# Performance work log

Measured on AMD Instinct MI355X. Metric: run time of the kernel, lower is better.

The kernel has to match this reference:

```python
import jax, jax.numpy as jnp
import numpy as np
from jax import lax

UP = 4          # upscale_factor (pixel_shuffle factor hardcoded to 4 in ReconBlock)
OUT_CH = UP * UP * 5 * 5  # 400
MID_CH = UP * 5           # 20


def setup_inputs() -> dict:
    key = jax.random.key(0)
    ks = jax.random.split(key, 5)
    B, A, H, W = 2, 5, 96, 96
    pic = jax.random.uniform(ks[0], (B, A, A, H, W), dtype=jnp.float32)
    w1 = jax.random.normal(ks[1], (OUT_CH, 1, 5, 5, 9, 9), dtype=jnp.float32) * 0.02
    b1 = jnp.zeros((OUT_CH,), jnp.float32)
    w2a = jax.random.normal(ks[2], (MID_CH, 1, 3, 3, 5, 5), dtype=jnp.float32) * 0.02
    b2a = jnp.zeros((MID_CH,), jnp.float32)
    w2b = jax.random.normal(ks[3], (OUT_CH, MID_CH, 3, 3, 5, 5), dtype=jnp.float32) * 0.02
    b2b = jnp.zeros((OUT_CH,), jnp.float32)
    return {"pic": pic, "w1": w1, "b1": b1, "w2a": w2a, "b2a": b2a,
            "w2b": w2b, "b2b": b2b}


def _conv4d(x, w):
    # x: [B, Cin, A1, A2, H, W], w: [Cout, Cin, k1, k2, k3, k4], VALID, stride 1
    return lax.conv_general_dilated(x, w, window_strides=(1, 1, 1, 1),
                                    padding='VALID')


def _bias(b):
    return b[None, :, None, None, None, None]


def reference(pic, w1, b1, w2a, b2a, w2b, b2b):
    B, A1, A2, H, W = pic.shape
    # Padder: pad H,W by 4 each side with value 0.5
    padded = jnp.full((B, A1, A2, H + 8, W + 8), 0.5, dtype=pic.dtype)
    padded = padded.at[:, :, :, 4:-4, 4:-4].set(pic)
    x = padded[:, None]  # [B,1,A1,A2,H+8,W+8]

    # DimBlock_1: single 4D conv (5,5,9,9); ReLU defined but never applied
    p1 = _conv4d(x, w1) + _bias(b1)              # [B,400,1,1,H,W]

    # DimBlock_2: two 4D convs (3,3,5,5) with ReLU
    buf = jax.nn.relu(_conv4d(x, w2a) + _bias(b2a))   # [B,20,3,3,H+4,W+4]
    p2 = jax.nn.relu(_conv4d(buf, w2b) + _bias(b2b))  # [B,400,1,1,H,W]

    # BottleNeck
    mid = (p1 + p2) / 2                           # [B,400,1,1,H,W]

    # ReconBlock: take angular position (0,0), pixel_shuffle(4), split 25 -> 5x5
    y = mid[:, :, 0, 0]                           # [B,400,H,W]
    Bc, C, Hh, Ww = y.shape
    r = 4
    y = y.reshape(Bc, 25, r, r, Hh, Ww)
    y = y.transpose(0, 1, 4, 2, 5, 3).reshape(Bc, 25, Hh * r, Ww * r)
    return y.reshape(Bc, 5, 5, Hh * r, Ww * r)
```

## Files before the change

kernel.cpp:

```cpp
#include <hip/hip_runtime.h>
#include <hip/hip_bf16.h>


typedef __attribute__((ext_vector_type(8))) unsigned short ushort8;
typedef __attribute__((ext_vector_type(8))) __bf16 bf16x8;
typedef __attribute__((ext_vector_type(4))) float f32x4;

#define NB 2
#define HSLOT 576
#define HBUF (4 * HSLOT * 8)
#define WST 14336

static __device__ __forceinline__ unsigned short f2bf(float f) {
    __hip_bfloat16 h = __float2bfloat16(f);
    return *reinterpret_cast<unsigned short*>(&h);
}
static __device__ __forceinline__ void gload16(const unsigned short* g, unsigned short* l) {
    __builtin_amdgcn_global_load_lds(
        (const __attribute__((address_space(1))) unsigned int*)(const void*)g,
        (__attribute__((address_space(3))) unsigned int*)(void*)l, 16, 0, 0);
}

__global__ __launch_bounds__(256) void prep_fused_kernel(
    const float* __restrict__ pic, const float* __restrict__ w1,
    const float* __restrict__ w2a, const float* __restrict__ w2b,
    unsigned short* __restrict__ Pn, unsigned short* __restrict__ Wp,
    unsigned short* __restrict__ Wc2) {
    __shared__ unsigned short sT[28544];
    const int blk = blockIdx.x;
    const int tid = threadIdx.x;

    if (blk < 85) {
        int idx = blk * 256 + tid;
        if (idx >= NB * 104 * 104) return;
        int x = idx % 104;
        int y = (idx / 104) % 104;
        int b = idx / (104 * 104);
        unsigned short vals[32];
        bool inter = (y >= 4 && y < 100 && x >= 4 && x < 100);
#pragma unroll
        for (int c = 0; c < 25; ++c) {
            float v = inter ? pic[((b * 25 + c) * 96 + (y - 4)) * 96 + (x - 4)] : 0.5f;
            vals[c] = f2bf(v);
        }
#pragma unroll
        for (int c = 25; c < 32; ++c) vals[c] = 0;
        ushort8* dst = (ushort8*)(Pn + idx * 32);
#pragma unroll
        for (int j = 0; j < 4; ++j) dst[j] = *(ushort8*)&vals[j * 8];
    } else if (blk < 127) {
        int b2 = blk - 85;
        int ocB = b2 % 7, cc = b2 / 7;
        for (int n32 = 0; n32 < 2; ++n32) {
            for (int j = 0; j < 4; ++j) {
                int p  = tid * 4 + j;
                int gl = p >> 5, ol = p & 31;
                int oc = ocB * 64 + n32 * 32 + ol;
                int gp = cc * 32 + gl;
                const float* src = nullptr;
                if (oc < 400 && gp < 180) {
                    int mc = gp % 20, uv = gp / 20;
                    src = w2b + oc * 4500 + (mc * 9 + uv) * 25;
                }
#pragma unroll
                for (int tap = 0; tap < 25; ++tap)
                    sT[(gl * 25 + tap) * 33 + ol] = src ? f2bf(src[tap]) : (unsigned short)0;
            }
            __syncthreads();
            for (int i = 0; i < 13; ++i) {
                int sid = i * 256 + tid;
                if (sid < 3200) {
                    int tap = sid >> 7;
                    int r   = sid & 127;
                    int nb = r >> 6, lane = r & 63;
                    int kq = lane >> 4;
                    int olw = nb * 16 + (lane & 15);
                    unsigned short v8[8];
#pragma unroll
                    for (int e = 0; e < 8; ++e)
                        v8[e] = sT[((kq * 8 + e) * 25 + tap) * 33 + olw];
                    size_t d = (size_t)(cc * 25 + tap) * WST + ocB * 2048 +
                               (n32 * 2 + nb) * 512 + lane * 8;
                    *(ushort8*)(Wp + d) = *(ushort8*)v8;
                }
            }
            __syncthreads();
        }
    } else if (blk < 148) {
        int b3 = blk - 127;
        int ocB = b3 % 7, tt = b3 / 7;
        for (int n32 = 0; n32 < 2; ++n32) {
            for (int j = 0; j < 4; ++j) {
                int p  = tid * 4 + j;
                int cl = p >> 5, ol = p & 31;
                int oc = ocB * 64 + n32 * 32 + ol;
                const float* src = (oc < 400 && cl < 25)
                                       ? (w1 + oc * 2025 + cl * 81 + tt * 27) : nullptr;
#pragma unroll
                for (int tl = 0; tl < 27; ++tl)
                    sT[(cl * 27 + tl) * 33 + ol] = src ? f2bf(src[tl]) : (unsigned short)0;
            }
            __syncthreads();
            for (int i = 0; i < 14; ++i) {
                int sid = i * 256 + tid;
                if (sid < 3456) {
                    int tl = sid >> 7;
                    int r  = sid & 127;
                    int nb = r >> 6, lane = r & 63;
                    int kq = lane >> 4;
                    int olw = nb * 16 + (lane & 15);
                    unsigned short v8[8];
#pragma unroll
                    for (int e = 0; e < 8; ++e)
                        v8[e] = sT[((kq * 8 + e) * 27 + tl) * 33 + olw];
                    int tap_lin = tt * 27 + tl;
                    int dy = tap_lin / 9, dx = tap_lin % 9;
                    int tp = (dx < 5) ? (dy * 5 + dx) : (45 + dy * 4 + (dx - 5));
                    size_t d = (size_t)(150 + tp) * WST + ocB * 2048 +
                               (n32 * 2 + nb) * 512 + lane * 8;
                    *(ushort8*)(Wp + d) = *(ushort8*)v8;
                }
            }
            __syncthreads();
        }
    } else if (blk < 154) {
        int ocB2 = blk - 148;
        if (tid < 128) {
            int lane = tid & 63;
            int oc = ocB2 * 32 + (tid >> 6) * 16 + (lane & 15);
            int kb = (lane >> 4) * 8;
            int uv = oc / 20, mc = oc % 20;
            int u = uv / 3, v = uv % 3;
            const float* wb[8];
#pragma unroll
            for (int e = 0; e < 8; ++e) {
                int k  = kb + e;
                int c1 = k / 5, c2 = k % 5;
                int da1 = c1 - u, da2 = c2 - v;
                bool valid = (oc < 180) && ((unsigned)da1 < 3u) && ((unsigned)da2 < 3u);
                wb[e] = valid ? (w2a + mc * 225 + (da1 * 3 + da2) * 25) : (const float*)0;
            }
            for (int tap = 0; tap < 25; ++tap) {
                unsigned short fr[8];
#pragma unroll
                for (int e = 0; e < 8; ++e) fr[e] = wb[e] ? f2bf(wb[e][tap]) : (unsigned short)0;
                *(ushort8*)(Wc2 + ((size_t)(ocB2 * 25 + tap) * 128 + tid) * 8) = *(ushort8*)fr;
            }
        }
    }
}

__global__ __launch_bounds__(256) void conv2a_mfma_kernel(
    const unsigned short* __restrict__ Pn, const unsigned short* __restrict__ Wc2,
    const float* __restrict__ b2a, unsigned short* __restrict__ Bn) {
    __shared__ __align__(16) unsigned short sHalo[4 * 448 * 8];

    const int tid  = threadIdx.x;
    const int lane = tid & 63, w = tid >> 6;
    const int l15  = lane & 15, lhi = lane >> 4;
    const int gx0  = blockIdx.x;
    const int b    = gx0 / 52, t52 = gx0 % 52;
    const int ty0  = (t52 >> 2) * 8;
    const int tx0  = (t52 & 3) * 32;
    const int ocB  = blockIdx.y;

    for (int L2 = 0; L2 < 7; ++L2) {
        int p = L2 * 64 + lane;
        if (p >= 432) p = 0;
        int hy = (p * 58255) >> 21, hx = p - hy * 36;
        int gy = ty0 + hy; gy = gy > 103 ? 103 : gy;
        int gx = tx0 + hx; gx = gx > 103 ? 103 : gx;
        gload16(Pn + ((size_t)((b * 104 + gy) * 104 + gx)) * 32 + w * 8,
                &sHalo[(w * 448 + L2 * 64) * 8]);
    }
    float bs[2];
#pragma unroll
    for (int n = 0; n < 2; ++n) {
        int oc = ocB * 32 + n * 16 + l15;
        bs[n] = (oc < 180) ? b2a[oc % 20] : 0.f;
    }
    __syncthreads();

    const unsigned short* hb = &sHalo[(lhi * 448 + w * 72 + l15) * 8];
    const unsigned short* wq = Wc2 + (size_t)ocB * 25600 + lane * 8;

    f32x4 acc[4][2] = {};
#pragma unroll
    for (int t = 0; t < 25; ++t) {
        const int u = ((t / 5) * 36 + (t % 5)) * 8;
        bf16x8 a0 = *(const bf16x8*)(hb + u);
        bf16x8 a1 = *(const bf16x8*)(hb + u + 128);
        bf16x8 a2 = *(const bf16x8*)(hb + u + 288);
        bf16x8 a3 = *(const bf16x8*)(hb + u + 416);
        bf16x8 c0 = *(const bf16x8*)(wq);
        bf16x8 c1 = *(const bf16x8*)(wq + 512);
        __builtin_amdgcn_s_setprio(1);
        acc[0][0] = __builtin_amdgcn_mfma_f32_16x16x32_bf16(a0, c0, acc[0][0], 0, 0, 0);
        acc[0][1] = __builtin_amdgcn_mfma_f32_16x16x32_bf16(a0, c1, acc[0][1], 0, 0, 0);
        acc[1][0] = __builtin_amdgcn_mfma_f32_16x16x32_bf16(a1, c0, acc[1][0], 0, 0, 0);
        acc[1][1] = __builtin_amdgcn_mfma_f32_16x16x32_bf16(a1, c1, acc[1][1], 0, 0, 0);
        acc[2][0] = __builtin_amdgcn_mfma_f32_16x16x32_bf16(a2, c0, acc[2][0], 0, 0, 0);
        acc[2][1] = __builtin_amdgcn_mfma_f32_16x16x32_bf16(a2, c1, acc[2][1], 0, 0, 0);
        acc[3][0] = __builtin_amdgcn_mfma_f32_16x16x32_bf16(a3, c0, acc[3][0], 0, 0, 0);
        acc[3][1] = __builtin_amdgcn_mfma_f32_16x16x32_bf16(a3, c1, acc[3][1], 0, 0, 0);
        __builtin_amdgcn_s_setprio(0);
        wq += 1024;
    }

#pragma unroll
    for (int n = 0; n < 2; ++n) {
        int oc = ocB * 32 + n * 16 + l15;
#pragma unroll
        for (int m = 0; m < 4; ++m) {
            int y = ty0 + w * 2 + (m >> 1);
            if (y >= 100) continue;
            int x0 = tx0 + (m & 1) * 16 + lhi * 4;
#pragma unroll
            for (int i = 0; i < 4; ++i) {
                int x = x0 + i;
                if (x >= 100) continue;
                Bn[((size_t)((b * 100 + y) * 100 + x)) * 192 + oc] =
                    f2bf(fmaxf(acc[m][n][i] + bs[n], 0.f));
            }
        }
    }
}

#define MFMA16(A0, A1, A2, A3, B0, B1, B2, B3)                                          \
    {                                                                                   \
        __builtin_amdgcn_s_setprio(1);                                                  \
        acc[0][0] = __builtin_amdgcn_mfma_f32_16x16x32_bf16(A0, B0, acc[0][0], 0, 0, 0);\
        acc[0][1] = __builtin_amdgcn_mfma_f32_16x16x32_bf16(A0, B1, acc[0][1], 0, 0, 0);\
        acc[0][2] = __builtin_amdgcn_mfma_f32_16x16x32_bf16(A0, B2, acc[0][2], 0, 0, 0);\
        acc[0][3] = __builtin_amdgcn_mfma_f32_16x16x32_bf16(A0, B3, acc[0][3], 0, 0, 0);\
        acc[1][0] = __builtin_amdgcn_mfma_f32_16x16x32_bf16(A1, B0, acc[1][0], 0, 0, 0);\
        acc[1][1] = __builtin_amdgcn_mfma_f32_16x16x32_bf16(A1, B1, acc[1][1], 0, 0, 0);\
        acc[1][2] = __builtin_amdgcn_mfma_f32_16x16x32_bf16(A1, B2, acc[1][2], 0, 0, 0);\
        acc[1][3] = __builtin_amdgcn_mfma_f32_16x16x32_bf16(A1, B3, acc[1][3], 0, 0, 0);\
        acc[2][0] = __builtin_amdgcn_mfma_f32_16x16x32_bf16(A2, B0, acc[2][0], 0, 0, 0);\
        acc[2][1] = __builtin_amdgcn_mfma_f32_16x16x32_bf16(A2, B1, acc[2][1], 0, 0, 0);\
        acc[2][2] = __builtin_amdgcn_mfma_f32_16x16x32_bf16(A2, B2, acc[2][2], 0, 0, 0);\
        acc[2][3] = __builtin_amdgcn_mfma_f32_16x16x32_bf16(A2, B3, acc[2][3], 0, 0, 0);\
        acc[3][0] = __builtin_amdgcn_mfma_f32_16x16x32_bf16(A3, B0, acc[3][0], 0, 0, 0);\
        acc[3][1] = __builtin_amdgcn_mfma_f32_16x16x32_bf16(A3, B1, acc[3][1], 0, 0, 0);\
        acc[3][2] = __builtin_amdgcn_mfma_f32_16x16x32_bf16(A3, B2, acc[3][2], 0, 0, 0);\
        acc[3][3] = __builtin_amdgcn_mfma_f32_16x16x32_bf16(A3, B3, acc[3][3], 0, 0, 0);\
        __builtin_amdgcn_s_setprio(0);                                                  \
    }

__global__ __launch_bounds__(256, 2) void conv_mfma_kernel(
    const unsigned short* __restrict__ Pn, const unsigned short* __restrict__ Bn,
    const unsigned short* __restrict__ Wp, const float* __restrict__ b1,
    const float* __restrict__ b2b, float* __restrict__ out) {
    __shared__ __align__(16) unsigned short sHalo[2 * HBUF];

    const int tid  = threadIdx.x;
    const int lane = tid & 63, w = tid >> 6;
    const int l15  = lane & 15, lhi = lane >> 4;
    const int ocB  = blockIdx.y;
    const int pb   = blockIdx.x;
    const int b    = pb / 36;
    const int t36  = pb % 36;
    const int ty0  = (t36 / 3) * 8;
    const int tx0  = (t36 % 3) * 32;

    const int vA = (lhi * HSLOT + w * 72 + l15) * 8;

    auto stageA = [&](int cc, int par) {
        unsigned short* dst0 = &sHalo[par * HBUF + w * HSLOT * 8];
        for (int L2 = 0; L2 < 7; ++L2) {
            int p = L2 * 64 + lane;
            if (p >= 432) p = 0;
            int hy = (p * 58255) >> 21, hx = p - hy * 36;
            gload16(Bn + ((size_t)((b * 100 + ty0 + hy) * 100 + tx0 + hx)) * 192 +
                        cc * 32 + w * 8,
                    dst0 + L2 * 512);
        }
    };
    auto stageB = [&](int seg, int par) {
        int cx = tx0 + (seg == 7 ? 5 : 0);
        unsigned short* dst0 = &sHalo[par * HBUF + w * HSLOT * 8];
        for (int L2 = 0; L2 < 9; ++L2) {
            int p = L2 * 64 + lane;
            int hy = (p * 58255) >> 21, hx = p - hy * 36;
            int gx = cx + hx;
            gx = gx > 103 ? 103 : gx;
            gload16(Pn + ((size_t)((b * 104 + ty0 + hy) * 104 + gx)) * 32 + w * 8,
                    dst0 + L2 * 512);
        }
    };

    float bb2[4], bb1[4];
#pragma unroll
    for (int n = 0; n < 4; ++n) {
        int oc  = ocB * 64 + n * 16 + l15;
        int occ = oc < 400 ? oc : 399;
        bb2[n] = b2b[occ];
        bb1[n] = b1[occ];
    }

    const unsigned short* wq = Wp + ocB * 2048 + lane * 8;
    bf16x8 c0 = *(const bf16x8*)(wq);
    bf16x8 c1 = *(const bf16x8*)(wq + 512);
    bf16x8 c2 = *(const bf16x8*)(wq + 1024);
    bf16x8 c3 = *(const bf16x8*)(wq + 1536);
    stageA(0, 0);
    __syncthreads();

    f32x4 acc[4][4] = {};
    bf16x8 a0, a1, a2, a3, q0, q1, q2, q3, n0, n1, n2, n3;

    for (int cc = 0; cc < 6; ++cc) {
        const unsigned short* hb = &sHalo[(cc & 1) * HBUF + vA];
        a0 = *(const bf16x8*)(hb);
        a1 = *(const bf16x8*)(hb + 128);
        a2 = *(const bf16x8*)(hb + 288);
        a3 = *(const bf16x8*)(hb + 416);
        if (cc < 5) stageA(cc + 1, (cc + 1) & 1);
        else        stageB(6, 0);
#pragma unroll
        for (int t = 0; t < 25; ++t) {
            wq += WST;
            n0 = *(const bf16x8*)(wq);
            n1 = *(const bf16x8*)(wq + 512);
            n2 = *(const bf16x8*)(wq + 1024);
            n3 = *(const bf16x8*)(wq + 1536);
            if (t < 24) {
                const int u = (((t + 1) / 5) * 36 + ((t + 1) % 5)) * 8;
                q0 = *(const bf16x8*)(hb + u);
                q1 = *(const bf16x8*)(hb + u + 128);
                q2 = *(const bf16x8*)(hb + u + 288);
                q3 = *(const bf16x8*)(hb + u + 416);
            }
            MFMA16(a0, a1, a2, a3, c0, c1, c2, c3);
            c0 = n0; c1 = n1; c2 = n2; c3 = n3;
            if (t < 24) { a0 = q0; a1 = q1; a2 = q2; a3 = q3; }
        }
        if (cc == 5) {
#pragma unroll
            for (int m = 0; m < 4; ++m)
#pragma unroll
                for (int n = 0; n < 4; ++n)
#pragma unroll
                    for (int i = 0; i < 4; ++i)
                        acc[m][n][i] = fmaxf(acc[m][n][i] + bb2[n], 0.f);
        }
        asm volatile("s_waitcnt vmcnt(4)" ::: "memory");
        asm volatile("s_barrier" ::: "memory");
    }

    {
        const unsigned short* hb = &sHalo[vA];
        a0 = *(const bf16x8*)(hb);
        a1 = *(const bf16x8*)(hb + 128);
        a2 = *(const bf16x8*)(hb + 288);
        a3 = *(const bf16x8*)(hb + 416);
        stageB(7, 1);
#pragma unroll
        for (int t = 0; t < 45; ++t) {
            wq += WST;
            n0 = *(const bf16x8*)(wq);
            n1 = *(const bf16x8*)(wq + 512);
            n2 = *(const bf16x8*)(wq + 1024);
            n3 = *(const bf16x8*)(wq + 1536);
            if (t < 44) {
                const int u = (((t + 1) / 5) * 36 + ((t + 1) % 5)) * 8;
                q0 = *(const bf16x8*)(hb + u);
                q1 = *(const bf16x8*)(hb + u + 128);
                q2 = *(const bf16x8*)(hb + u + 288);
                q3 = *(const bf16x8*)(hb + u + 416);
            }
            MFMA16(a0, a1, a2, a3, c0, c1, c2, c3);
            c0 = n0; c1 = n1; c2 = n2; c3 = n3;
            if (t < 44) { a0 = q0; a1 = q1; a2 = q2; a3 = q3; }
        }
        asm volatile("s_waitcnt vmcnt(4)" ::: "memory");
        asm volatile("s_barrier" ::: "memory");
    }

    {
        const unsigned short* hb = &sHalo[HBUF + vA];
        a0 = *(const bf16x8*)(hb);
        a1 = *(const bf16x8*)(hb + 128);
        a2 = *(const bf16x8*)(hb + 288);
        a3 = *(const bf16x8*)(hb + 416);
#pragma unroll
        for (int t = 0; t < 36; ++t) {
            if (t < 35) {
                wq += WST;
                n0 = *(const bf16x8*)(wq);
                n1 = *(const bf16x8*)(wq + 512);
                n2 = *(const bf16x8*)(wq + 1024);
                n3 = *(const bf16x8*)(wq + 1536);
                const int u = (((t + 1) / 4) * 36 + ((t + 1) % 4)) * 8;
                q0 = *(const bf16x8*)(hb + u);
                q1 = *(const bf16x8*)(hb + u + 128);
                q2 = *(const bf16x8*)(hb + u + 288);
                q3 = *(const bf16x8*)(hb + u + 416);
            }
            MFMA16(a0, a1, a2, a3, c0, c1, c2, c3);
            if (t < 35) { a0 = q0; a1 = q1; a2 = q2; a3 = q3;
                          c0 = n0; c1 = n1; c2 = n2; c3 = n3; }
        }
    }

#pragma unroll
    for (int n = 0; n < 4; ++n) {
        int oc = ocB * 64 + n * 16 + l15;
        if (oc >= 400) continue;
        float bv = bb1[n];
        int c25 = oc >> 4, r1 = (oc >> 2) & 3, r2 = oc & 3;
#pragma unroll
        for (int m = 0; m < 4; ++m) {
            int y  = ty0 + w * 2 + (m >> 1);
            int x0 = tx0 + (m & 1) * 16 + lhi * 4;
#pragma unroll
            for (int i = 0; i < 4; ++i) {
                out[((size_t)(b * 25 + c25) * 384 + y * 4 + r1) * 384 + (x0 + i) * 4 + r2] =
                    (acc[m][n][i] + bv) * 0.5f;
            }
        }
    }
}

extern "C" void kernel_launch(void* const* d_in, const int* in_sizes, int n_in,
                              void* d_out, int out_size, void* d_ws, size_t ws_size,
                              hipStream_t stream) {
    const float* pic = (const float*)d_in[0];
    const float* w1  = (const float*)d_in[1];
    const float* b1  = (const float*)d_in[2];
    const float* w2a = (const float*)d_in[3];
    const float* b2a = (const float*)d_in[4];
    const float* w2b = (const float*)d_in[5];
    const float* b2b = (const float*)d_in[6];
    float* out = (float*)d_out;

    char* ws = (char*)d_ws;
    unsigned short* Pn  = (unsigned short*)(ws);
    unsigned short* Bn  = (unsigned short*)(ws + 1384448);
    unsigned short* Wp  = (unsigned short*)(ws + 9064448);
    unsigned short* Wc2 = (unsigned short*)(ws + 15687680);

    prep_fused_kernel<<<154, 256, 0, stream>>>(pic, w1, w2a, w2b, Pn, Wp, Wc2);
    conv2a_mfma_kernel<<<dim3(104, 6), 256, 0, stream>>>(Pn, Wc2, b2a, Bn);
    conv_mfma_kernel<<<dim3(72, 7), 256, 0, stream>>>(Pn, Bn, Wp, b1, b2b, out);
}
```

Measured before the change: 149.2 us.

## Move big weight repacking into conv2a launch to overlap with conv2a compute

The w2b and w1 weight repacking moves out of the prep kernel and into extra blocks of the conv2a kernel, so the prep kernel only handles the input padding and the small w2a repack. The repack blocks now process 16 output channels per pass with a smaller shared buffer, which lets them share LDS with the conv2a halo tile. The intent is to shorten the serial prep stage and run the weight transform alongside the conv2a MFMA work. The cost is a heterogeneous kernel whose repack blocks may take longer than the conv blocks and so set the tail.

Result: slower. 159.4 us (+6.8%).

```diff
diff --git a/kernel.cpp b/kernel.cpp
--- a/kernel.cpp
+++ b/kernel.cpp
@@ -21,15 +21,11 @@
         (__attribute__((address_space(3))) unsigned int*)(void*)l, 16, 0, 0);
 }
 
-__global__ __launch_bounds__(256) void prep_fused_kernel(
-    const float* __restrict__ pic, const float* __restrict__ w1,
-    const float* __restrict__ w2a, const float* __restrict__ w2b,
-    unsigned short* __restrict__ Pn, unsigned short* __restrict__ Wp,
-    unsigned short* __restrict__ Wc2) {
-    __shared__ unsigned short sT[28544];
+__global__ __launch_bounds__(256) void prep1_kernel(
+    const float* __restrict__ pic, const float* __restrict__ w2a,
+    unsigned short* __restrict__ Pn, unsigned short* __restrict__ Wc2) {
     const int blk = blockIdx.x;
     const int tid = threadIdx.x;
-
     if (blk < 85) {
         int idx = blk * 256 + tid;
         if (idx >= NB * 104 * 104) return;
@@ -48,83 +44,8 @@
         ushort8* dst = (ushort8*)(Pn + idx * 32);
 #pragma unroll
         for (int j = 0; j < 4; ++j) dst[j] = *(ushort8*)&vals[j * 8];
-    } else if (blk < 127) {
-        int b2 = blk - 85;
-        int ocB = b2 % 7, cc = b2 / 7;
-        for (int n32 = 0; n32 < 2; ++n32) {
-            for (int j = 0; j < 4; ++j) {
-                int p  = tid * 4 + j;
-                int gl = p >> 5, ol = p & 31;
-                int oc = ocB * 64 + n32 * 32 + ol;
-                int gp = cc * 32 + gl;
-                const float* src = nullptr;
-                if (oc < 400 && gp < 180) {
-                    int mc = gp % 20, uv = gp / 20;
-                    src = w2b + oc * 4500 + (mc * 9 + uv) * 25;
-                }
-#pragma unroll
-                for (int tap = 0; tap < 25; ++tap)
-                    sT[(gl * 25 + tap) * 33 + ol] = src ? f2bf(src[tap]) : (unsigned short)0;
-            }
-            __syncthreads();
-            for (int i = 0; i < 13; ++i) {
-                int sid = i * 256 + tid;
-                if (sid < 3200) {
-                    int tap = sid >> 7;
-                    int r   = sid & 127;
-                    int nb = r >> 6, lane = r & 63;
-                    int kq = lane >> 4;
-                    int olw = nb * 16 + (lane & 15);
-                    unsigned short v8[8];
-#pragma unroll
-                    for (int e = 0; e < 8; ++e)
-                        v8[e] = sT[((kq * 8 + e) * 25 + tap) * 33 + olw];
-                    size_t d = (size_t)(cc * 25 + tap) * WST + ocB * 2048 +
-                               (n32 * 2 + nb) * 512 + lane * 8;
-                    *(ushort8*)(Wp + d) = *(ushort8*)v8;
-                }
-            }
-            __syncthreads();
-        }
-    } else if (blk < 148) {
-        int b3 = blk - 127;
-        int ocB = b3 % 7, tt = b3 / 7;
-        for (int n32 = 0; n32 < 2; ++n32) {
-            for (int j = 0; j < 4; ++j) {
-                int p  = tid * 4 + j;
-                int cl = p >> 5, ol = p & 31;
-                int oc = ocB * 64 + n32 * 32 + ol;
-                const float* src = (oc < 400 && cl < 25)
-                                       ? (w1 + oc * 2025 + cl * 81 + tt * 27) : nullptr;
-#pragma unroll
-                for (int tl = 0; tl < 27; ++tl)
-                    sT[(cl * 27 + tl) * 33 + ol] = src ? f2bf(src[tl]) : (unsigned short)0;
-            }
-            __syncthreads();
-            for (int i = 0; i < 14; ++i) {
-                int sid = i * 256 + tid;
-                if (sid < 3456) {
-                    int tl = sid >> 7;
-                    int r  = sid & 127;
-                    int nb = r >> 6, lane = r & 63;
-                    int kq = lane >> 4;
-                    int olw = nb * 16 + (lane & 15);
-                    unsigned short v8[8];
-#pragma unroll
-                    for (int e = 0; e < 8; ++e)
-                        v8[e] = sT[((kq * 8 + e) * 27 + tl) * 33 + olw];
-                    int tap_lin = tt * 27 + tl;
-                    int dy = tap_lin / 9, dx = tap_lin % 9;
-                    int tp = (dx < 5) ? (dy * 5 + dx) : (45 + dy * 4 + (dx - 5));
-                    size_t d = (size_t)(150 + tp) * WST + ocB * 2048 +
-                               (n32 * 2 + nb) * 512 + lane * 8;
-                    *(ushort8*)(Wp + d) = *(ushort8*)v8;
-                }
-            }
-            __syncthreads();
-        }
-    } else if (blk < 154) {
-        int ocB2 = blk - 148;
+    } else {
+        int ocB2 = blk - 85;
         if (tid < 128) {
             int lane = tid & 63;
             int oc = ocB2 * 32 + (tid >> 6) * 16 + (lane & 15);
@@ -150,77 +71,153 @@
     }
 }
 
-__global__ __launch_bounds__(256) void conv2a_mfma_kernel(
+__global__ __launch_bounds__(256) void conv2a_fused_kernel(
     const unsigned short* __restrict__ Pn, const unsigned short* __restrict__ Wc2,
-    const float* __restrict__ b2a, unsigned short* __restrict__ Bn) {
-    __shared__ __align__(16) unsigned short sHalo[4 * 448 * 8];
-
-    const int tid  = threadIdx.x;
-    const int lane = tid & 63, w = tid >> 6;
-    const int l15  = lane & 15, lhi = lane >> 4;
-    const int gx0  = blockIdx.x;
-    const int b    = gx0 / 52, t52 = gx0 % 52;
-    const int ty0  = (t52 >> 2) * 8;
-    const int tx0  = (t52 & 3) * 32;
-    const int ocB  = blockIdx.y;
-
-    for (int L2 = 0; L2 < 7; ++L2) {
-        int p = L2 * 64 + lane;
-        if (p >= 432) p = 0;
-        int hy = (p * 58255) >> 21, hx = p - hy * 36;
-        int gy = ty0 + hy; gy = gy > 103 ? 103 : gy;
-        int gx = tx0 + hx; gx = gx > 103 ? 103 : gx;
-        gload16(Pn + ((size_t)((b * 104 + gy) * 104 + gx)) * 32 + w * 8,
-                &sHalo[(w * 448 + L2 * 64) * 8]);
-    }
-    float bs[2];
-#pragma unroll
-    for (int n = 0; n < 2; ++n) {
-        int oc = ocB * 32 + n * 16 + l15;
-        bs[n] = (oc < 180) ? b2a[oc % 20] : 0.f;
-    }
-    __syncthreads();
-
-    const unsigned short* hb = &sHalo[(lhi * 448 + w * 72 + l15) * 8];
-    const unsigned short* wq = Wc2 + (size_t)ocB * 25600 + lane * 8;
-
-    f32x4 acc[4][2] = {};
-#pragma unroll
-    for (int t = 0; t < 25; ++t) {
-        const int u = ((t / 5) * 36 + (t % 5)) * 8;
-        bf16x8 a0 = *(const bf16x8*)(hb + u);
-        bf16x8 a1 = *(const bf16x8*)(hb + u + 128);
-        bf16x8 a2 = *(const bf16x8*)(hb + u + 288);
-        bf16x8 a3 = *(const bf16x8*)(hb + u + 416);
-        bf16x8 c0 = *(const bf16x8*)(wq);
-        bf16x8 c1 = *(const bf16x8*)(wq + 512);
-        __builtin_amdgcn_s_setprio(1);
-        acc[0][0] = __builtin_amdgcn_mfma_f32_16x16x32_bf16(a0, c0, acc[0][0], 0, 0, 0);
-        acc[0][1] = __builtin_amdgcn_mfma_f32_16x16x32_bf16(a0, c1, acc[0][1], 0, 0, 0);
-        acc[1][0] = __builtin_amdgcn_mfma_f32_16x16x32_bf16(a1, c0, acc[1][0], 0, 0, 0);
-        acc[1][1] = __builtin_amdgcn_mfma_f32_16x16x32_bf16(a1, c1, acc[1][1], 0, 0, 0);
-        acc[2][0] = __builtin_amdgcn_mfma_f32_16x16x32_bf16(a2, c0, acc[2][0], 0, 0, 0);
-        acc[2][1] = __builtin_amdgcn_mfma_f32_16x16x32_bf16(a2, c1, acc[2][1], 0, 0, 0);
-        acc[3][0] = __builtin_amdgcn_mfma_f32_16x16x32_bf16(a3, c0, acc[3][0], 0, 0, 0);
-        acc[3][1] = __builtin_amdgcn_mfma_f32_16x16x32_bf16(a3, c1, acc[3][1], 0, 0, 0);
-        __builtin_amdgcn_s_setprio(0);
-        wq += 1024;
-    }
-
-#pragma unroll
-    for (int n = 0; n < 2; ++n) {
-        int oc = ocB * 32 + n * 16 + l15;
-#pragma unroll
-        for (int m = 0; m < 4; ++m) {
-            int y = ty0 + w * 2 + (m >> 1);
-            if (y >= 100) continue;
-            int x0 = tx0 + (m & 1) * 16 + lhi * 4;
-#pragma unroll
-            for (int i = 0; i < 4; ++i) {
-                int x = x0 + i;
-                if (x >= 100) continue;
-                Bn[((size_t)((b * 100 + y) * 100 + x)) * 192 + oc] =
-                    f2bf(fmaxf(acc[m][n][i] + bs[n], 0.f));
+    const float* __restrict__ b2a, const float* __restrict__ w1,
+    const float* __restrict__ w2b, unsigned short* __restrict__ Bn,
+    unsigned short* __restrict__ Wp) {
+    __shared__ __align__(16) unsigned short sMem[14336];
+    const int bx  = blockIdx.x;
+    const int tid = threadIdx.x;
+
+    if (bx < 42) {
+        int ocB = bx % 7, cc = bx / 7;
+        for (int n32 = 0; n32 < 4; ++n32) {
+            if (n32) __syncthreads();
+#pragma unroll
+            for (int j = 0; j < 2; ++j) {
+                int p  = tid * 2 + j;
+                int gl = p >> 4, ol = p & 15;
+                int oc = ocB * 64 + n32 * 16 + ol;
+                int gp = cc * 32 + gl;
+                const float* src = nullptr;
+                if (oc < 400 && gp < 180) {
+                    int mc = gp % 20, uv = gp / 20;
+                    src = w2b + oc * 4500 + (mc * 9 + uv) * 25;
+                }
+                for (int tap = 0; tap < 25; ++tap)
+                    sMem[(gl * 25 + tap) * 17 + ol] = src ? f2bf(src[tap]) : (unsigned short)0;
+            }
+            __syncthreads();
+            for (int i = 0; i < 7; ++i) {
+                int sid = i * 256 + tid;
+                if (sid < 1600) {
+                    int tap = sid >> 6, lane = sid & 63;
+                    int kq = lane >> 4, l15 = lane & 15;
+                    unsigned short v8[8];
+#pragma unroll
+                    for (int e = 0; e < 8; ++e)
+                        v8[e] = sMem[((kq * 8 + e) * 25 + tap) * 17 + l15];
+                    size_t d = (size_t)(cc * 25 + tap) * WST + ocB * 2048 + n32 * 512 + lane * 8;
+                    *(ushort8*)(Wp + d) = *(ushort8*)v8;
+                }
+            }
+        }
+    } else if (bx < 63) {
+        int b3 = bx - 42;
+        int ocB = b3 % 7, tt = b3 / 7;
+        for (int n32 = 0; n32 < 4; ++n32) {
+            if (n32) __syncthreads();
+#pragma unroll
+            for (int j = 0; j < 2; ++j) {
+                int p  = tid * 2 + j;
+                int cl = p >> 4, ol = p & 15;
+                if (cl < 25) {
+                    int oc = ocB * 64 + n32 * 16 + ol;
+                    const float* src = (oc < 400) ? (w1 + oc * 2025 + cl * 81 + tt * 27)
+                                                  : (const float*)0;
+                    for (int tl = 0; tl < 27; ++tl)
+                        sMem[(cl * 27 + tl) * 17 + ol] = src ? f2bf(src[tl]) : (unsigned short)0;
+                }
+            }
+            __syncthreads();
+            for (int i = 0; i < 7; ++i) {
+                int sid = i * 256 + tid;
+                if (sid < 1728) {
+                    int tl = sid >> 6, lane = sid & 63;
+                    int kq = lane >> 4, l15 = lane & 15;
+                    unsigned short v8[8];
+#pragma unroll
+                    for (int e = 0; e < 8; ++e) {
+                        int k = kq * 8 + e;
+                        v8[e] = (k < 25) ? sMem[(k * 27 + tl) * 17 + l15] : (unsigned short)0;
+                    }
+                    int tap_lin = tt * 27 + tl;
+                    int dy = tap_lin / 9, dx = tap_lin % 9;
+                    int tp = (dx < 5) ? (dy * 5 + dx) : (45 + dy * 4 + (dx - 5));
+                    size_t d = (size_t)(150 + tp) * WST + ocB * 2048 + n32 * 512 + lane * 8;
+                    *(ushort8*)(Wp + d) = *(ushort8*)v8;
+                }
+            }
+        }
+    } else {
+        int cid = bx - 63;
+        const int lane = tid & 63, w = tid >> 6;
+        const int l15  = lane & 15, lhi = lane >> 4;
+        const int gx0  = cid % 104;
+        const int ocB  = cid / 104;
+        const int b    = gx0 / 52, t52 = gx0 % 52;
+        const int ty0  = (t52 >> 2) * 8;
+        const int tx0  = (t52 & 3) * 32;
+
+        for (int L2 = 0; L2 < 7; ++L2) {
+            int p = L2 * 64 + lane;
+            if (p >= 432) p = 0;
+            int hy = (p * 58255) >> 21, hx = p - hy * 36;
+            int gy = ty0 + hy; gy = gy > 103 ? 103 : gy;
+            int gx = tx0 + hx; gx = gx > 103 ? 103 : gx;
+            gload16(Pn + ((size_t)((b * 104 + gy) * 104 + gx)) * 32 + w * 8,
+                    &sMem[(w * 448 + L2 * 64) * 8]);
+        }
+        float bs[2];
+#pragma unroll
+        for (int n = 0; n < 2; ++n) {
+            int oc = ocB * 32 + n * 16 + l15;
+            bs[n] = (oc < 180) ? b2a[oc % 20] : 0.f;
+        }
+        __syncthreads();
+
+        const unsigned short* hb = &sMem[(lhi * 448 + w * 72 + l15) * 8];
+        const unsigned short* wq = Wc2 + (size_t)ocB * 25600 + lane * 8;
+
+        f32x4 acc[4][2] = {};
+#pragma unroll
+        for (int t = 0; t < 25; ++t) {
+            const int u = ((t / 5) * 36 + (t % 5)) * 8;
+            bf16x8 a0 = *(const bf16x8*)(hb + u);
+            bf16x8 a1 = *(const bf16x8*)(hb + u + 128);
+            bf16x8 a2 = *(const bf16x8*)(hb + u + 288);
+            bf16x8 a3 = *(const bf16x8*)(hb + u + 416);
+            bf16x8 c0 = *(const bf16x8*)(wq);
+            bf16x8 c1 = *(const bf16x8*)(wq + 512);
+            __builtin_amdgcn_s_setprio(1);
+            acc[0][0] = __builtin_amdgcn_mfma_f32_16x16x32_bf16(a0, c0, acc[0][0], 0, 0, 0);
+            acc[0][1] = __builtin_amdgcn_mfma_f32_16x16x32_bf16(a0, c1, acc[0][1], 0, 0, 0);
+            acc[1][0] = __builtin_amdgcn_mfma_f32_16x16x32_bf16(a1, c0, acc[1][0], 0, 0, 0);
+            acc[1][1] = __builtin_amdgcn_mfma_f32_16x16x32_bf16(a1, c1, acc[1][1], 0, 0, 0);
+            acc[2][0] = __builtin_amdgcn_mfma_f32_16x16x32_bf16(a2, c0, acc[2][0], 0, 0, 0);
+            acc[2][1] = __builtin_amdgcn_mfma_f32_16x16x32_bf16(a2, c1, acc[2][1], 0, 0, 0);
+            acc[3][0] = __builtin_amdgcn_mfma_f32_16x16x32_bf16(a3, c0, acc[3][0], 0, 0, 0);
+            acc[3][1] = __builtin_amdgcn_mfma_f32_16x16x32_bf16(a3, c1, acc[3][1], 0, 0, 0);
+            __builtin_amdgcn_s_setprio(0);
+            wq += 1024;
+        }
+
+#pragma unroll
+        for (int n = 0; n < 2; ++n) {
+            int oc = ocB * 32 + n * 16 + l15;
+#pragma unroll
+            for (int m = 0; m < 4; ++m) {
+                int y = ty0 + w * 2 + (m >> 1);
+                if (y >= 100) continue;
+                int x0 = tx0 + (m & 1) * 16 + lhi * 4;
+#pragma unroll
+                for (int i = 0; i < 4; ++i) {
+                    int x = x0 + i;
+                    if (x >= 100) continue;
+                    Bn[((size_t)((b * 100 + y) * 100 + x)) * 192 + oc] =
+                        f2bf(fmaxf(acc[m][n][i] + bs[n], 0.f));
+                }
             }
         }
     }
@@ -441,7 +438,7 @@
     unsigned short* Wp  = (unsigned short*)(ws + 9064448);
     unsigned short* Wc2 = (unsigned short*)(ws + 15687680);
 
-    prep_fused_kernel<<<154, 256, 0, stream>>>(pic, w1, w2a, w2b, Pn, Wp, Wc2);
-    conv2a_mfma_kernel<<<dim3(104, 6), 256, 0, stream>>>(Pn, Wc2, b2a, Bn);
+    prep1_kernel<<<91, 256, 0, stream>>>(pic, w2a, Pn, Wc2);
+    conv2a_fused_kernel<<<687, 256, 0, stream>>>(Pn, Wc2, b2a, w1, w2b, Bn, Wp);
     conv_mfma_kernel<<<dim3(72, 7), 256, 0, stream>>>(Pn, Bn, Wp, b1, b2b, out);
 }
```
